# Performance work log

Measured on AMD Instinct MI355X. Metric: run time of the kernel, lower is better.

The kernel has to match this reference:

```python
import jax, jax.numpy as jnp
import numpy as np

EPS = 1e-8  # torch CosineSimilarity default eps

def setup_inputs() -> dict:
    key = jax.random.key(0)
    kv, kt, k1, k2, k3, k4 = jax.random.split(key, 6)
    B, S = 16, 1024
    VD, TD, H = 1024, 768, 512
    visual_features = jax.random.normal(kv, (B, S, VD), dtype=jnp.float32)
    text_features = jax.random.normal(kt, (B, S, TD), dtype=jnp.float32)
    # nn.Linear params: weight [out, in], bias [out]
    Wv = jax.random.normal(k1, (H, VD), dtype=jnp.float32) * (1.0 / np.sqrt(VD))
    bv = jax.random.normal(k2, (H,), dtype=jnp.float32) * 0.01
    Wt = jax.random.normal(k3, (H, TD), dtype=jnp.float32) * (1.0 / np.sqrt(TD))
    bt = jax.random.normal(k4, (H,), dtype=jnp.float32) * 0.01
    return {"visual_features": visual_features, "text_features": text_features,
            "Wv": Wv, "bv": bv, "Wt": Wt, "bt": bt}

def reference(visual_features, text_features, Wv, bv, Wt, bt):
    # Linear projections
    v = jnp.einsum('bsd,hd->bsh', visual_features, Wv) + bv  # [B,S,H]
    t = jnp.einsum('bsd,hd->bsh', text_features, Wt) + bt    # [B,S,H]
    # Cosine similarity matrix via normalized batched GEMM
    # (algebraically equal to broadcasting CosineSimilarity over (B,S,S,H))
    dots = jnp.einsum('bih,bjh->bij', v, t)                   # [B,S,S]
    vn = jnp.linalg.norm(v, axis=-1)                          # [B,S]
    tn = jnp.linalg.norm(t, axis=-1)                          # [B,S]
    denom = jnp.maximum(vn[:, :, None] * tn[:, None, :], EPS)
    return dots / denom
```

## Files before the change

kernel.cpp:

```cpp
#include <hip/hip_runtime.h>
#include <hip/hip_bf16.h>

typedef __bf16 bf16x8 __attribute__((ext_vector_type(8)));
typedef __bf16 bf16x4 __attribute__((ext_vector_type(4)));
typedef float  f32x4  __attribute__((ext_vector_type(4)));

#define MFMA16(a, b, c) __builtin_amdgcn_mfma_f32_16x16x32_bf16((a), (b), (c), 0, 0, 0)

#define BATCH 16
#define SEQ   1024
#define VD    1024
#define TD    768
#define HDIM  512
#define MROWS (BATCH * SEQ)

typedef __attribute__((address_space(1))) const unsigned int gas_uint;
typedef __attribute__((address_space(3))) unsigned int las_uint;

__device__ __forceinline__ void async_copy16(const void* g, void* l) {
    __builtin_amdgcn_global_load_lds((gas_uint*)g, (las_uint*)l, 16, 0, 0);
}

__device__ __forceinline__ void stage_tile_bf16(const __bf16* __restrict__ src,
                                                size_t ld, int row0, int k0,
                                                __bf16* __restrict__ buf, int tid) {
#pragma unroll
    for (int i = 0; i < 4; ++i) {
        const int c = i * 256 + tid;
        const int r = c >> 3;
        const int g = (c & 7) ^ (r & 7);
        async_copy16(&src[(size_t)(row0 + r) * ld + k0 + g * 8],
                     &buf[(c & ~63) * 8]);
    }
}

__device__ __forceinline__ void stage_tile256(const __bf16* __restrict__ src,
                                              size_t ld, int row0, int k0,
                                              __bf16* __restrict__ buf, int tid) {
#pragma unroll
    for (int i = 0; i < 4; ++i) {
        const int c = i * 512 + tid;
        const int r = c >> 3;
        const int g = (c & 7) ^ (r & 7);
        async_copy16(&src[(size_t)(row0 + r) * ld + k0 + g * 8],
                     &buf[(c & ~63) * 8]);
    }
}

__device__ __forceinline__ bf16x8 frag_read(const __bf16* __restrict__ buf,
                                            int r, int h, int fq) {
    return *reinterpret_cast<const bf16x8*>(&buf[(r * 8 + ((h * 4 + fq) ^ (r & 7))) * 8]);
}

#define NC_XV (BATCH * SEQ * VD / 4)
#define NC_XT (BATCH * SEQ * TD / 4)
#define NC_WV (HDIM * VD / 4)
#define NC_WT (HDIM * TD / 4)
#define NC_TOTAL (NC_XV + NC_XT + NC_WV + NC_WT)

__global__ __launch_bounds__(256) void conv_kernel(
    const float* __restrict__ Xv, const float* __restrict__ Xt,
    const float* __restrict__ Wv, const float* __restrict__ Wt,
    __bf16* __restrict__ Xvb, __bf16* __restrict__ Xtb,
    __bf16* __restrict__ Wvb, __bf16* __restrict__ Wtb) {
    int i = blockIdx.x * 256 + threadIdx.x;
    if (i >= NC_TOTAL) return;
    const float* src;
    __bf16* dst;
    if (i < NC_XV)                     { src = Xv; dst = Xvb; }
    else if ((i -= NC_XV) < NC_XT)     { src = Xt; dst = Xtb; }
    else if ((i -= NC_XT) < NC_WV)     { src = Wv; dst = Wvb; }
    else { i -= NC_WV;                   src = Wt; dst = Wtb; }
    const float4 x = reinterpret_cast<const float4*>(src)[i];
    bf16x4 p = {(__bf16)x.x, (__bf16)x.y, (__bf16)x.z, (__bf16)x.w};
    reinterpret_cast<bf16x4*>(dst)[i] = p;
}

__global__ __launch_bounds__(256) void proj_kernel(
    const __bf16* __restrict__ Xvb, const __bf16* __restrict__ Wvb, const float* __restrict__ bv_,
    const __bf16* __restrict__ Xtb, const __bf16* __restrict__ Wtb, const float* __restrict__ bt_,
    __bf16* __restrict__ vout, __bf16* __restrict__ tout,
    float* __restrict__ vn2, float* __restrict__ tn2)
{
    const int L     = blockIdx.x;
    const int mlow  = L & 7;
    const int n     = (L >> 3) & 3;
    const int mhigh = (L >> 5) & 15;
    const int z     = L >> 9;
    const int m0    = (mhigh * 8 + mlow) * 128;
    const int n0    = n * 128;

    const __bf16* X; const __bf16* Wb; const float* bias; __bf16* out; float* n2; int K;
    if (z == 0) { X = Xvb; Wb = Wvb; bias = bv_; out = vout; n2 = vn2; K = VD; }
    else        { X = Xtb; Wb = Wtb; bias = bt_; out = tout; n2 = tn2; K = TD; }

    __shared__ __bf16 As[2][128 * 64];
    __shared__ __bf16 Bs[2][128 * 64];

    const int tid  = threadIdx.x;
    const int lane = tid & 63;
    const int wave = tid >> 6;
    const int wr   = wave >> 1;
    const int wc   = wave & 1;
    const int fr   = lane & 15;
    const int fq   = lane >> 4;

    f32x4 acc[4][4] = {};
    const int nk = K >> 6;

    stage_tile_bf16(X,  K, m0, 0, As[0], tid);
    stage_tile_bf16(Wb, K, n0, 0, Bs[0], tid);
    __syncthreads();

    for (int ki = 0; ki < nk; ++ki) {
        if (ki + 1 < nk) {
            const int kk = (ki + 1) << 6;
            stage_tile_bf16(X,  K, m0, kk, As[(ki + 1) & 1], tid);
            stage_tile_bf16(Wb, K, n0, kk, Bs[(ki + 1) & 1], tid);
        }
        const __bf16* Ab = As[ki & 1];
        const __bf16* Bb = Bs[ki & 1];
#pragma unroll
        for (int h = 0; h < 2; ++h) {
            bf16x8 a[4], b[4];
#pragma unroll
            for (int tm = 0; tm < 4; ++tm)
                a[tm] = frag_read(Ab, wr * 64 + tm * 16 + fr, h, fq);
#pragma unroll
            for (int tn = 0; tn < 4; ++tn)
                b[tn] = frag_read(Bb, wc * 64 + tn * 16 + fr, h, fq);
#pragma unroll
            for (int tm = 0; tm < 4; ++tm)
#pragma unroll
                for (int tn = 0; tn < 4; ++tn)
                    acc[tm][tn] = MFMA16(a[tm], b[tn], acc[tm][tn]);
        }
        __syncthreads();
    }

    float bc[4];
#pragma unroll
    for (int tn = 0; tn < 4; ++tn)
        bc[tn] = bias[n0 + wc * 64 + tn * 16 + fr];

#pragma unroll
    for (int tm = 0; tm < 4; ++tm) {
        const int rowb = m0 + wr * 64 + tm * 16 + fq * 4;
#pragma unroll
        for (int r = 0; r < 4; ++r) {
            float s = 0.f;
#pragma unroll
            for (int tn = 0; tn < 4; ++tn) {
                const float e = acc[tm][tn][r] + bc[tn];
                out[(size_t)(rowb + r) * HDIM + n0 + wc * 64 + tn * 16 + fr] = (__bf16)e;
                s = fmaf(e, e, s);
            }
            s += __shfl_xor(s, 1);
            s += __shfl_xor(s, 2);
            s += __shfl_xor(s, 4);
            s += __shfl_xor(s, 8);
            if (fr == 0) atomicAdd(&n2[rowb + r], s);
        }
    }
}

__global__ __launch_bounds__(512, 2) void dots_kernel(const __bf16* __restrict__ v,
                                                      const __bf16* __restrict__ t,
                                                      const float* __restrict__ vn2,
                                                      const float* __restrict__ tn2,
                                                      float* __restrict__ out) {
    __shared__ __bf16 As[2][256 * 64];
    __shared__ __bf16 Bs[2][256 * 64];

    const int L  = blockIdx.x;
    const int x  = L & 7;
    const int s  = L >> 3;
    const int b  = x * 2 + (s >> 4);
    const int i0 = ((s >> 2) & 3) * 256;
    const int j0 = (s & 3) * 256;

    const __bf16* vb = v + (size_t)b * SEQ * HDIM;
    const __bf16* tb = t + (size_t)b * SEQ * HDIM;

    const int tid  = threadIdx.x;
    const int lane = tid & 63;
    const int wave = tid >> 6;
    const int wr   = wave >> 2;
    const int wc   = wave & 3;
    const int fr   = lane & 15;
    const int fq   = lane >> 4;

    f32x4 acc[8][4] = {};
    const int NKT = HDIM >> 6;

    stage_tile256(vb, HDIM, i0, 0,  As[0], tid);
    stage_tile256(tb, HDIM, j0, 0,  Bs[0], tid);
    stage_tile256(vb, HDIM, i0, 64, As[1], tid);
    stage_tile256(tb, HDIM, j0, 64, Bs[1], tid);
    asm volatile("s_waitcnt vmcnt(8)" ::: "memory");
    __builtin_amdgcn_s_barrier();

    for (int kt = 0; kt < NKT; ++kt) {
        const __bf16* Ab = As[kt & 1];
        const __bf16* Bb = Bs[kt & 1];
        bf16x8 bfr[4][2];
#pragma unroll
        for (int q = 0; q < 4; ++q) {
            bf16x8 afr[2][2];
#pragma unroll
            for (int m2 = 0; m2 < 2; ++m2)
#pragma unroll
                for (int h = 0; h < 2; ++h)
                    afr[m2][h] = frag_read(Ab, wr * 128 + (q * 2 + m2) * 16 + fr, h, fq);
            if (q == 0) {
#pragma unroll
                for (int n = 0; n < 4; ++n)
#pragma unroll
                    for (int h = 0; h < 2; ++h)
                        bfr[n][h] = frag_read(Bb, wc * 64 + n * 16 + fr, h, fq);
            }
            __builtin_amdgcn_s_barrier();
            __builtin_amdgcn_s_setprio(1);
#pragma unroll
            for (int h = 0; h < 2; ++h)
#pragma unroll
                for (int m2 = 0; m2 < 2; ++m2)
#pragma unroll
                    for (int n = 0; n < 4; ++n)
                        acc[q * 2 + m2][n] = MFMA16(afr[m2][h], bfr[n][h], acc[q * 2 + m2][n]);
            __builtin_amdgcn_s_setprio(0);
        }
        if (kt < NKT - 1) {
            __builtin_amdgcn_s_barrier();
            __builtin_amdgcn_sched_barrier(0);
            if (kt + 2 < NKT) {
                const int kk = (kt + 2) << 6;
                stage_tile256(vb, HDIM, i0, kk, As[kt & 1], tid);
                stage_tile256(tb, HDIM, j0, kk, Bs[kt & 1], tid);
                asm volatile("s_waitcnt vmcnt(8)" ::: "memory");
            } else {
                asm volatile("s_waitcnt vmcnt(0)" ::: "memory");
            }
            __builtin_amdgcn_sched_barrier(0);
            __builtin_amdgcn_s_barrier();
        }
    }

    float vr2[8][4];
#pragma unroll
    for (int mf = 0; mf < 8; ++mf)
#pragma unroll
        for (int r = 0; r < 4; ++r)
            vr2[mf][r] = vn2[b * SEQ + i0 + wr * 128 + mf * 16 + fq * 4 + r];

    float* outb = out + ((size_t)b << 20);
#pragma unroll
    for (int n = 0; n < 4; ++n) {
        const int j     = j0 + wc * 64 + n * 16 + fr;
        const float tj2 = tn2[b * SEQ + j];
#pragma unroll
        for (int mf = 0; mf < 8; ++mf) {
            const int ib = i0 + wr * 128 + mf * 16 + fq * 4;
#pragma unroll
            for (int r = 0; r < 4; ++r) {
                const float denom = fmaxf(sqrtf(vr2[mf][r] * tj2), 1e-8f);
                outb[(size_t)(ib + r) * SEQ + j] = acc[mf][n][r] * __builtin_amdgcn_rcpf(denom);
            }
        }
    }
}

extern "C" void kernel_launch(void* const* d_in, const int* in_sizes, int n_in,
                              void* d_out, int out_size, void* d_ws, size_t ws_size,
                              hipStream_t stream) {
    const float* Xv = (const float*)d_in[0];
    const float* Xt = (const float*)d_in[1];
    const float* Wv = (const float*)d_in[2];
    const float* bv = (const float*)d_in[3];
    const float* Wt = (const float*)d_in[4];
    const float* bt = (const float*)d_in[5];
    float* out = (float*)d_out;

    char* ws = (char*)d_ws;
    size_t off = 0;
    __bf16* v   = (__bf16*)(ws + off); off += (size_t)MROWS * HDIM * 2;
    __bf16* t   = (__bf16*)(ws + off); off += (size_t)MROWS * HDIM * 2;
    __bf16* Xvb = (__bf16*)(ws + off); off += (size_t)MROWS * VD * 2;
    __bf16* Xtb = (__bf16*)(ws + off); off += (size_t)MROWS * TD * 2;
    __bf16* Wvb = (__bf16*)(ws + off); off += (size_t)HDIM * VD * 2;
    __bf16* Wtb = (__bf16*)(ws + off); off += (size_t)HDIM * TD * 2;
    float*  vn2 = (float*)(ws + off);  off += (size_t)MROWS * 4;
    float*  tn2 = (float*)(ws + off);  off += (size_t)MROWS * 4;

    hipMemsetAsync(vn2, 0, (size_t)2 * MROWS * 4, stream);

    conv_kernel<<<(NC_TOTAL + 255) / 256, 256, 0, stream>>>(Xv, Xt, Wv, Wt, Xvb, Xtb, Wvb, Wtb);

    proj_kernel<<<1024, 256, 0, stream>>>(Xvb, Wvb, bv, Xtb, Wtb, bt, v, t, vn2, tn2);

    dots_kernel<<<256, 512, 0, stream>>>(v, t, vn2, tn2, out);
}
```

Baseline: 236.9 us.

## Enlarge projection GEMM tiles to 256x256 with prefetch pipeline and grid-stride conversion

Result: slower. 248.8 us (+5.0%).

```diff
diff --git a/kernel.cpp b/kernel.cpp
--- a/kernel.cpp
+++ b/kernel.cpp
@@ -21,19 +21,6 @@
     __builtin_amdgcn_global_load_lds((gas_uint*)g, (las_uint*)l, 16, 0, 0);
 }
 
-__device__ __forceinline__ void stage_tile_bf16(const __bf16* __restrict__ src,
-                                                size_t ld, int row0, int k0,
-                                                __bf16* __restrict__ buf, int tid) {
-#pragma unroll
-    for (int i = 0; i < 4; ++i) {
-        const int c = i * 256 + tid;
-        const int r = c >> 3;
-        const int g = (c & 7) ^ (r & 7);
-        async_copy16(&src[(size_t)(row0 + r) * ld + k0 + g * 8],
-                     &buf[(c & ~63) * 8]);
-    }
-}
-
 __device__ __forceinline__ void stage_tile256(const __bf16* __restrict__ src,
                                               size_t ld, int row0, int k0,
                                               __bf16* __restrict__ buf, int tid) {
@@ -57,109 +44,147 @@
 #define NC_WV (HDIM * VD / 4)
 #define NC_WT (HDIM * TD / 4)
 #define NC_TOTAL (NC_XV + NC_XT + NC_WV + NC_WT)
+#define CONV_ITERS   32
+#define CONV_THREADS (NC_TOTAL / CONV_ITERS)
+#define CONV_BLOCKS  (CONV_THREADS / 256)
 
 __global__ __launch_bounds__(256) void conv_kernel(
     const float* __restrict__ Xv, const float* __restrict__ Xt,
     const float* __restrict__ Wv, const float* __restrict__ Wt,
     __bf16* __restrict__ Xvb, __bf16* __restrict__ Xtb,
     __bf16* __restrict__ Wvb, __bf16* __restrict__ Wtb) {
-    int i = blockIdx.x * 256 + threadIdx.x;
-    if (i >= NC_TOTAL) return;
-    const float* src;
-    __bf16* dst;
-    if (i < NC_XV)                     { src = Xv; dst = Xvb; }
-    else if ((i -= NC_XV) < NC_XT)     { src = Xt; dst = Xtb; }
-    else if ((i -= NC_XT) < NC_WV)     { src = Wv; dst = Wvb; }
-    else { i -= NC_WV;                   src = Wt; dst = Wtb; }
-    const float4 x = reinterpret_cast<const float4*>(src)[i];
-    bf16x4 p = {(__bf16)x.x, (__bf16)x.y, (__bf16)x.z, (__bf16)x.w};
-    reinterpret_cast<bf16x4*>(dst)[i] = p;
-}
-
-__global__ __launch_bounds__(256) void proj_kernel(
+    const int t0 = blockIdx.x * 256 + threadIdx.x;
+#pragma unroll
+    for (int g = 0; g < CONV_ITERS / 4; ++g) {
+        float4 x[4];
+        int kk[4];
+        __bf16* dd[4];
+#pragma unroll
+        for (int u = 0; u < 4; ++u) {
+            int k = t0 + (g * 4 + u) * CONV_THREADS;
+            const float* src;
+            if (k < NC_XV)                 { src = Xv; dd[u] = Xvb; }
+            else if ((k -= NC_XV) < NC_XT) { src = Xt; dd[u] = Xtb; }
+            else if ((k -= NC_XT) < NC_WV) { src = Wv; dd[u] = Wvb; }
+            else { k -= NC_WV;               src = Wt; dd[u] = Wtb; }
+            kk[u] = k;
+            x[u] = reinterpret_cast<const float4*>(src)[k];
+        }
+#pragma unroll
+        for (int u = 0; u < 4; ++u) {
+            bf16x4 p = {(__bf16)x[u].x, (__bf16)x[u].y, (__bf16)x[u].z, (__bf16)x[u].w};
+            reinterpret_cast<bf16x4*>(dd[u])[kk[u]] = p;
+        }
+    }
+}
+
+__global__ __launch_bounds__(512, 2) void proj_kernel(
     const __bf16* __restrict__ Xvb, const __bf16* __restrict__ Wvb, const float* __restrict__ bv_,
     const __bf16* __restrict__ Xtb, const __bf16* __restrict__ Wtb, const float* __restrict__ bt_,
     __bf16* __restrict__ vout, __bf16* __restrict__ tout,
     float* __restrict__ vn2, float* __restrict__ tn2)
 {
-    const int L     = blockIdx.x;
-    const int mlow  = L & 7;
-    const int n     = (L >> 3) & 3;
-    const int mhigh = (L >> 5) & 15;
-    const int z     = L >> 9;
-    const int m0    = (mhigh * 8 + mlow) * 128;
-    const int n0    = n * 128;
+    __shared__ __bf16 As[2][256 * 64];
+    __shared__ __bf16 Bs[2][256 * 64];
+
+    const int L  = blockIdx.x;
+    const int x  = L & 7;
+    const int s  = L >> 3;
+    const int z  = s >> 4;
+    const int ss = s & 15;
+    const int m0 = (x * 8 + (ss >> 1)) * 256;
+    const int n0 = (ss & 1) * 256;
 
     const __bf16* X; const __bf16* Wb; const float* bias; __bf16* out; float* n2; int K;
     if (z == 0) { X = Xvb; Wb = Wvb; bias = bv_; out = vout; n2 = vn2; K = VD; }
     else        { X = Xtb; Wb = Wtb; bias = bt_; out = tout; n2 = tn2; K = TD; }
 
-    __shared__ __bf16 As[2][128 * 64];
-    __shared__ __bf16 Bs[2][128 * 64];
-
     const int tid  = threadIdx.x;
     const int lane = tid & 63;
     const int wave = tid >> 6;
-    const int wr   = wave >> 1;
-    const int wc   = wave & 1;
+    const int wr   = wave >> 2;
+    const int wc   = wave & 3;
     const int fr   = lane & 15;
     const int fq   = lane >> 4;
 
-    f32x4 acc[4][4] = {};
-    const int nk = K >> 6;
-
-    stage_tile_bf16(X,  K, m0, 0, As[0], tid);
-    stage_tile_bf16(Wb, K, n0, 0, Bs[0], tid);
-    __syncthreads();
-
-    for (int ki = 0; ki < nk; ++ki) {
-        if (ki + 1 < nk) {
-            const int kk = (ki + 1) << 6;
-            stage_tile_bf16(X,  K, m0, kk, As[(ki + 1) & 1], tid);
-            stage_tile_bf16(Wb, K, n0, kk, Bs[(ki + 1) & 1], tid);
-        }
-        const __bf16* Ab = As[ki & 1];
-        const __bf16* Bb = Bs[ki & 1];
-#pragma unroll
-        for (int h = 0; h < 2; ++h) {
-            bf16x8 a[4], b[4];
-#pragma unroll
-            for (int tm = 0; tm < 4; ++tm)
-                a[tm] = frag_read(Ab, wr * 64 + tm * 16 + fr, h, fq);
-#pragma unroll
-            for (int tn = 0; tn < 4; ++tn)
-                b[tn] = frag_read(Bb, wc * 64 + tn * 16 + fr, h, fq);
-#pragma unroll
-            for (int tm = 0; tm < 4; ++tm)
-#pragma unroll
-                for (int tn = 0; tn < 4; ++tn)
-                    acc[tm][tn] = MFMA16(a[tm], b[tn], acc[tm][tn]);
-        }
-        __syncthreads();
+    f32x4 acc[8][4] = {};
+    const int NKT = K >> 6;
+
+    stage_tile256(X,  K, m0, 0,  As[0], tid);
+    stage_tile256(Wb, K, n0, 0,  Bs[0], tid);
+    stage_tile256(X,  K, m0, 64, As[1], tid);
+    stage_tile256(Wb, K, n0, 64, Bs[1], tid);
+    asm volatile("s_waitcnt vmcnt(8)" ::: "memory");
+    __builtin_amdgcn_s_barrier();
+
+    for (int kt = 0; kt < NKT; ++kt) {
+        const __bf16* Ab = As[kt & 1];
+        const __bf16* Bb = Bs[kt & 1];
+        bf16x8 bfr[4][2];
+#pragma unroll
+        for (int q = 0; q < 4; ++q) {
+            bf16x8 afr[2][2];
+#pragma unroll
+            for (int m2 = 0; m2 < 2; ++m2)
+#pragma unroll
+                for (int h = 0; h < 2; ++h)
+                    afr[m2][h] = frag_read(Ab, wr * 128 + (q * 2 + m2) * 16 + fr, h, fq);
+            if (q == 0) {
+#pragma unroll
+                for (int n = 0; n < 4; ++n)
+#pragma unroll
+                    for (int h = 0; h < 2; ++h)
+                        bfr[n][h] = frag_read(Bb, wc * 64 + n * 16 + fr, h, fq);
+            }
+            __builtin_amdgcn_s_barrier();
+            __builtin_amdgcn_s_setprio(1);
+#pragma unroll
+            for (int h = 0; h < 2; ++h)
+#pragma unroll
+                for (int m2 = 0; m2 < 2; ++m2)
+#pragma unroll
+                    for (int n = 0; n < 4; ++n)
+                        acc[q * 2 + m2][n] = MFMA16(afr[m2][h], bfr[n][h], acc[q * 2 + m2][n]);
+            __builtin_amdgcn_s_setprio(0);
+        }
+        if (kt < NKT - 1) {
+            __builtin_amdgcn_s_barrier();
+            __builtin_amdgcn_sched_barrier(0);
+            if (kt + 2 < NKT) {
+                const int kk = (kt + 2) << 6;
+                stage_tile256(X,  K, m0, kk, As[kt & 1], tid);
+                stage_tile256(Wb, K, n0, kk, Bs[kt & 1], tid);
+                asm volatile("s_waitcnt vmcnt(8)" ::: "memory");
+            } else {
+                asm volatile("s_waitcnt vmcnt(0)" ::: "memory");
+            }
+            __builtin_amdgcn_sched_barrier(0);
+            __builtin_amdgcn_s_barrier();
+        }
     }
 
     float bc[4];
 #pragma unroll
-    for (int tn = 0; tn < 4; ++tn)
-        bc[tn] = bias[n0 + wc * 64 + tn * 16 + fr];
-
-#pragma unroll
-    for (int tm = 0; tm < 4; ++tm) {
-        const int rowb = m0 + wr * 64 + tm * 16 + fq * 4;
+    for (int n = 0; n < 4; ++n)
+        bc[n] = bias[n0 + wc * 64 + n * 16 + fr];
+
+#pragma unroll
+    for (int mf = 0; mf < 8; ++mf) {
+        const int rowb = m0 + wr * 128 + mf * 16 + fq * 4;
 #pragma unroll
         for (int r = 0; r < 4; ++r) {
-            float s = 0.f;
-#pragma unroll
-            for (int tn = 0; tn < 4; ++tn) {
-                const float e = acc[tm][tn][r] + bc[tn];
-                out[(size_t)(rowb + r) * HDIM + n0 + wc * 64 + tn * 16 + fr] = (__bf16)e;
-                s = fmaf(e, e, s);
-            }
-            s += __shfl_xor(s, 1);
-            s += __shfl_xor(s, 2);
-            s += __shfl_xor(s, 4);
-            s += __shfl_xor(s, 8);
-            if (fr == 0) atomicAdd(&n2[rowb + r], s);
+            float s_ = 0.f;
+#pragma unroll
+            for (int n = 0; n < 4; ++n) {
+                const float e = acc[mf][n][r] + bc[n];
+                out[(size_t)(rowb + r) * HDIM + n0 + wc * 64 + n * 16 + fr] = (__bf16)e;
+                s_ = fmaf(e, e, s_);
+            }
+            s_ += __shfl_xor(s_, 1);
+            s_ += __shfl_xor(s_, 2);
+            s_ += __shfl_xor(s_, 4);
+            s_ += __shfl_xor(s_, 8);
+            if (fr == 0) atomicAdd(&n2[rowb + r], s_);
         }
     }
 }
@@ -294,9 +319,9 @@
 
     hipMemsetAsync(vn2, 0, (size_t)2 * MROWS * 4, stream);
 
-    conv_kernel<<<(NC_TOTAL + 255) / 256, 256, 0, stream>>>(Xv, Xt, Wv, Wt, Xvb, Xtb, Wvb, Wtb);
-
-    proj_kernel<<<1024, 256, 0, stream>>>(Xvb, Wvb, bv, Xtb, Wtb, bt, v, t, vn2, tn2);
+    conv_kernel<<<CONV_BLOCKS, 256, 0, stream>>>(Xv, Xt, Wv, Wt, Xvb, Xtb, Wvb, Wtb);
+
+    proj_kernel<<<256, 512, 0, stream>>>(Xvb, Wvb, bv, Xtb, Wtb, bt, v, t, vn2, tn2);
 
     dots_kernel<<<256, 512, 0, stream>>>(v, t, vn2, tn2, out);
 }
```
